# Optimization experiments

Measured on AMD Instinct MI355X. Metric: run time of the kernel, lower is better.

## Reference

```python
import jax, jax.numpy as jnp
import numpy as np

EPS = 1e-09  # present in module but unused in forward math

def setup_inputs() -> dict:
    key = jax.random.key(0)
    k1, k2 = jax.random.split(key)
    n, d = 4096, 512
    outputs = jax.random.normal(k1, (n, d), dtype=jnp.float32)
    labels = jax.random.randint(k2, (n,), 0, 100, dtype=jnp.int64)
    return {"outputs": outputs, "labels": labels, "margin": 1.0}

def reference(outputs, labels, margin):
    # Pairwise squared L2 distances D[i,j] = ||x_i - x_j||^2 via expansion.
    sq = jnp.sum(outputs * outputs, axis=-1)                     # [n]
    D = sq[:, None] + sq[None, :] - 2.0 * (outputs @ outputs.T)  # [n, n]
    D = jnp.maximum(D, 0.0)
    same = (labels[:, None] == labels[None, :])                  # [n, n] bool; includes diagonal
    zn1 = jnp.sum(same)
    zn2 = same.size - zn1
    sum1 = jnp.sum(jnp.where(same, D, 0.0))
    sum2 = jnp.sum(jnp.where(same, 0.0, jnp.maximum(0.0, margin - D)))
    return 0.5 * (sum1 / zn1 + sum2 / zn2)
```

## Files before the change

kernel.cpp:

```cpp
#include <hip/hip_runtime.h>
#include <stdint.h>

#define NROWS 4096
#define DIM   512
#define BK    32
#define TILE  128
#define NBLK  32
#define NPAIR 528

typedef float f32x4 __attribute__((ext_vector_type(4)));
typedef short s16x8 __attribute__((ext_vector_type(8)));

#define OFF_XB   0u
#define OFF_SQ   (NROWS * DIM * 2u)
#define OFF_LAB  (OFF_SQ + NROWS * 4u)
#define OFF_ACC  (OFF_LAB + NROWS * 4u)

__device__ __forceinline__ unsigned short f2bf(float f) {
  unsigned u = __float_as_uint(f);
  return (unsigned short)((u + 0x7FFFu + ((u >> 16) & 1u)) >> 16);
}

typedef __attribute__((address_space(1))) unsigned int glb_uint;
typedef __attribute__((address_space(3))) unsigned int lds_uint;

__device__ __forceinline__ void gl2lds16(const void* g, void* l) {
  __builtin_amdgcn_global_load_lds(
      (glb_uint*)(uintptr_t)g,
      (lds_uint*)(unsigned int)(uintptr_t)l,
      16, 0, 0);
}

__global__ __launch_bounds__(256) void prep_kernel(
    const float* __restrict__ X, const long long* __restrict__ lab,
    unsigned short* __restrict__ Xb, float* __restrict__ sq,
    int* __restrict__ labi, float* __restrict__ accum)
{
  int t = threadIdx.x;
  int gid = blockIdx.x * 256 + t;
  if (gid < 4) accum[gid] = 0.0f;
  if (gid < NROWS) labi[gid] = (int)lab[gid];

  int wave = t >> 6, lane = t & 63;
  int row = blockIdx.x * 4 + wave;
  const float4* Xr = (const float4*)(X + (size_t)row * DIM);
  float4 a = Xr[lane * 2];
  float4 b = Xr[lane * 2 + 1];

  uint4 pk;
  pk.x = (unsigned)f2bf(a.x) | ((unsigned)f2bf(a.y) << 16);
  pk.y = (unsigned)f2bf(a.z) | ((unsigned)f2bf(a.w) << 16);
  pk.z = (unsigned)f2bf(b.x) | ((unsigned)f2bf(b.y) << 16);
  pk.w = (unsigned)f2bf(b.z) | ((unsigned)f2bf(b.w) << 16);
  *(uint4*)(Xb + (size_t)row * DIM + lane * 8) = pk;

  float s = a.x*a.x + a.y*a.y + a.z*a.z + a.w*a.w
          + b.x*b.x + b.y*b.y + b.z*b.z + b.w*b.w;
  #pragma unroll
  for (int off = 32; off; off >>= 1) s += __shfl_down(s, off, 64);
  if (lane == 0) sq[row] = s;
}

__global__ __launch_bounds__(256) void pair_kernel(
    const unsigned short* __restrict__ Xb, const float* __restrict__ sq,
    const int* __restrict__ labi, const float* __restrict__ marginp,
    float* __restrict__ accum)
{
  __shared__ unsigned short As[TILE * BK];
  __shared__ unsigned short Bs[TILE * BK];
  __shared__ float sRow[TILE], sCol[TILE];
  __shared__ int   lRow[TILE], lCol[TILE];
  __shared__ float rs1[4], rs2[4];
  __shared__ int   rc[4];

  int t = threadIdx.x;

  int rem = blockIdx.x, bi = 0;
  while (rem >= (NBLK - bi)) { rem -= (NBLK - bi); bi++; }
  int bj = bi + rem;

  int wave = t >> 6, lane = t & 63;
  int quad = lane >> 4, ml = lane & 15;
  int waveRow = (wave >> 1) * 64, waveCol = (wave & 1) * 64;

  f32x4 acc[4][4] = {};

  const int r0 = t >> 2;
  const int c0 = (t & 3) * 8;
  const size_t gA0 = (size_t)(bi * TILE +       r0) * DIM + c0;
  const size_t gA1 = (size_t)(bi * TILE + 64 +  r0) * DIM + c0;
  const size_t gB0 = (size_t)(bj * TILE +       r0) * DIM + c0;
  const size_t gB1 = (size_t)(bj * TILE + 64 +  r0) * DIM + c0;

  const s16x8* Ap = (const s16x8*)As;
  const s16x8* Bp = (const s16x8*)Bs;

  for (int kt = 0; kt < DIM / BK; ++kt) {
    __syncthreads();
    size_t ko = (size_t)kt * BK;
    gl2lds16(Xb + gA0 + ko, (void*)(As + t * 8));
    gl2lds16(Xb + gA1 + ko, (void*)(As + 2048 + t * 8));
    gl2lds16(Xb + gB0 + ko, (void*)(Bs + t * 8));
    gl2lds16(Xb + gB1 + ko, (void*)(Bs + 2048 + t * 8));
    __syncthreads();

    s16x8 af[4], bfr[4];
    #pragma unroll
    for (int r = 0; r < 4; ++r)
      af[r] = Ap[(waveRow + r * 16 + ml) * 4 + quad];
    #pragma unroll
    for (int c = 0; c < 4; ++c)
      bfr[c] = Bp[(waveCol + c * 16 + ml) * 4 + quad];

    #pragma unroll
    for (int r = 0; r < 4; ++r)
      #pragma unroll
      for (int c = 0; c < 4; ++c)
        acc[r][c] = __builtin_amdgcn_mfma_f32_16x16x32_bf16(af[r], bfr[c], acc[r][c], 0, 0, 0);
  }

  if (t < TILE) {
    sRow[t] = sq[bi * TILE + t];
    lRow[t] = labi[bi * TILE + t];
  } else {
    int u = t - TILE;
    sCol[u] = sq[bj * TILE + u];
    lCol[u] = labi[bj * TILE + u];
  }
  __syncthreads();

  float margin = *marginp;
  float s1 = 0.f, s2 = 0.f;
  int cnt = 0;
  #pragma unroll
  for (int c = 0; c < 4; ++c) {
    int col = waveCol + c * 16 + ml;
    float sqc = sCol[col];
    int lc = lCol[col];
    #pragma unroll
    for (int r = 0; r < 4; ++r) {
      int rbase = waveRow + r * 16 + quad * 4;
      #pragma unroll
      for (int i = 0; i < 4; ++i) {
        int row = rbase + i;
        float d = sRow[row] + sqc - 2.0f * acc[r][c][i];
        d = fmaxf(d, 0.0f);
        if (lRow[row] == lc) { s1 += d; cnt++; }
        else                 { s2 += fmaxf(margin - d, 0.0f); }
      }
    }
  }

  #pragma unroll
  for (int off = 32; off; off >>= 1) {
    s1  += __shfl_down(s1, off, 64);
    s2  += __shfl_down(s2, off, 64);
    cnt += __shfl_down(cnt, off, 64);
  }
  if (lane == 0) { rs1[wave] = s1; rs2[wave] = s2; rc[wave] = cnt; }
  __syncthreads();
  if (t == 0) {
    float f = (bi == bj) ? 1.f : 2.f;
    float S1 = 0.f, S2 = 0.f;
    int C = 0;
    for (int w = 0; w < 4; ++w) { S1 += rs1[w]; S2 += rs2[w]; C += rc[w]; }
    atomicAdd(&accum[0], S1 * f);
    atomicAdd(&accum[1], S2 * f);
    atomicAdd((unsigned*)accum + 2, (unsigned)C * (unsigned)((bi == bj) ? 1 : 2));
  }
}

__global__ void final_kernel(const float* __restrict__ accum, float* __restrict__ out) {
  unsigned c1 = ((const unsigned*)accum)[2];
  double zn1 = (double)c1;
  double zn2 = (double)NROWS * (double)NROWS - zn1;
  double res = 0.5 * ((double)accum[0] / zn1 + (double)accum[1] / zn2);
  out[0] = (float)res;
}

extern "C" void kernel_launch(void* const* d_in, const int* in_sizes, int n_in,
                              void* d_out, int out_size, void* d_ws, size_t ws_size,
                              hipStream_t stream) {
  const float*     X      = (const float*)d_in[0];
  const long long* lab    = (const long long*)d_in[1];
  const float*     margin = (const float*)d_in[2];
  float*           out    = (float*)d_out;

  char* ws = (char*)d_ws;
  unsigned short* Xb   = (unsigned short*)(ws + OFF_XB);
  float*          sq   = (float*)(ws + OFF_SQ);
  int*            labi = (int*)(ws + OFF_LAB);
  float*          accum= (float*)(ws + OFF_ACC);

  prep_kernel<<<NROWS / 4, 256, 0, stream>>>(X, lab, Xb, sq, labi, accum);
  pair_kernel<<<NPAIR, 256, 0, stream>>>(Xb, sq, labi, margin, accum);
  final_kernel<<<1, 1, 0, stream>>>(accum, out);
}
```

Measured before the change: 98.58 us.

## Double-buffer LDS tiles, swizzle LDS layout, fold final reduction into pair kernel

The pair kernel now double-buffers the A and B LDS tiles, so the global-to-LDS copy for the next K step is issued before the MFMAs on the current step. This drops one barrier per iteration and overlaps load latency with compute. An XOR swizzle on the 16-byte chunk index cuts LDS bank conflicts on fragment reads. The separate final kernel is removed: the last block to finish, detected with an atomic ticket counter, computes the output, which saves one launch at the cost of a threadfence and an extra atomic per block.

```diff
diff --git a/kernel.cpp b/kernel.cpp
--- a/kernel.cpp
+++ b/kernel.cpp
@@ -7,6 +7,7 @@
 #define TILE  128
 #define NBLK  32
 #define NPAIR 528
+#define KT    (DIM / BK)
 
 typedef float f32x4 __attribute__((ext_vector_type(4)));
 typedef short s16x8 __attribute__((ext_vector_type(8)));
@@ -64,10 +65,10 @@
 __global__ __launch_bounds__(256) void pair_kernel(
     const unsigned short* __restrict__ Xb, const float* __restrict__ sq,
     const int* __restrict__ labi, const float* __restrict__ marginp,
-    float* __restrict__ accum)
+    float* __restrict__ accum, float* __restrict__ out)
 {
-  __shared__ unsigned short As[TILE * BK];
-  __shared__ unsigned short Bs[TILE * BK];
+  __shared__ unsigned short As[2][TILE * BK];
+  __shared__ unsigned short Bs[2][TILE * BK];
   __shared__ float sRow[TILE], sCol[TILE];
   __shared__ int   lRow[TILE], lCol[TILE];
   __shared__ float rs1[4], rs2[4];
@@ -78,46 +79,6 @@
   int rem = blockIdx.x, bi = 0;
   while (rem >= (NBLK - bi)) { rem -= (NBLK - bi); bi++; }
   int bj = bi + rem;
-
-  int wave = t >> 6, lane = t & 63;
-  int quad = lane >> 4, ml = lane & 15;
-  int waveRow = (wave >> 1) * 64, waveCol = (wave & 1) * 64;
-
-  f32x4 acc[4][4] = {};
-
-  const int r0 = t >> 2;
-  const int c0 = (t & 3) * 8;
-  const size_t gA0 = (size_t)(bi * TILE +       r0) * DIM + c0;
-  const size_t gA1 = (size_t)(bi * TILE + 64 +  r0) * DIM + c0;
-  const size_t gB0 = (size_t)(bj * TILE +       r0) * DIM + c0;
-  const size_t gB1 = (size_t)(bj * TILE + 64 +  r0) * DIM + c0;
-
-  const s16x8* Ap = (const s16x8*)As;
-  const s16x8* Bp = (const s16x8*)Bs;
-
-  for (int kt = 0; kt < DIM / BK; ++kt) {
-    __syncthreads();
-    size_t ko = (size_t)kt * BK;
-    gl2lds16(Xb + gA0 + ko, (void*)(As + t * 8));
-    gl2lds16(Xb + gA1 + ko, (void*)(As + 2048 + t * 8));
-    gl2lds16(Xb + gB0 + ko, (void*)(Bs + t * 8));
-    gl2lds16(Xb + gB1 + ko, (void*)(Bs + 2048 + t * 8));
-    __syncthreads();
-
-    s16x8 af[4], bfr[4];
-    #pragma unroll
-    for (int r = 0; r < 4; ++r)
-      af[r] = Ap[(waveRow + r * 16 + ml) * 4 + quad];
-    #pragma unroll
-    for (int c = 0; c < 4; ++c)
-      bfr[c] = Bp[(waveCol + c * 16 + ml) * 4 + quad];
-
-    #pragma unroll
-    for (int r = 0; r < 4; ++r)
-      #pragma unroll
-      for (int c = 0; c < 4; ++c)
-        acc[r][c] = __builtin_amdgcn_mfma_f32_16x16x32_bf16(af[r], bfr[c], acc[r][c], 0, 0, 0);
-  }
 
   if (t < TILE) {
     sRow[t] = sq[bi * TILE + t];
@@ -127,7 +88,60 @@
     sCol[u] = sq[bj * TILE + u];
     lCol[u] = labi[bj * TILE + u];
   }
-  __syncthreads();
+
+  int wave = t >> 6, lane = t & 63;
+  int quad = lane >> 4, ml = lane & 15;
+  int waveRow = (wave >> 1) * 64, waveCol = (wave & 1) * 64;
+
+  f32x4 acc[4][4] = {};
+
+  const int r0 = t >> 2;
+  const int g  = (t & 3) ^ ((t >> 3) & 3);
+  const size_t gA0 = (size_t)(bi * TILE +      r0) * DIM + g * 8;
+  const size_t gA1 = (size_t)(bi * TILE + 64 + r0) * DIM + g * 8;
+  const size_t gB0 = (size_t)(bj * TILE +      r0) * DIM + g * 8;
+  const size_t gB1 = (size_t)(bj * TILE + 64 + r0) * DIM + g * 8;
+  const int ldst = t * 8;
+
+  const int slot = quad ^ ((ml >> 1) & 3);
+
+  gl2lds16(Xb + gA0, (void*)(As[0] + ldst));
+  gl2lds16(Xb + gA1, (void*)(As[0] + 2048 + ldst));
+  gl2lds16(Xb + gB0, (void*)(Bs[0] + ldst));
+  gl2lds16(Xb + gB1, (void*)(Bs[0] + 2048 + ldst));
+
+  for (int kt = 0; kt < KT; ++kt) {
+    int cur = kt & 1;
+    __syncthreads();
+
+    if (kt + 1 < KT) {
+      size_t ko = (size_t)(kt + 1) * BK;
+      gl2lds16(Xb + gA0 + ko, (void*)(As[cur ^ 1] + ldst));
+      gl2lds16(Xb + gA1 + ko, (void*)(As[cur ^ 1] + 2048 + ldst));
+      gl2lds16(Xb + gB0 + ko, (void*)(Bs[cur ^ 1] + ldst));
+      gl2lds16(Xb + gB1 + ko, (void*)(Bs[cur ^ 1] + 2048 + ldst));
+    }
+
+    const s16x8* Ap = (const s16x8*)As[cur];
+    const s16x8* Bp = (const s16x8*)Bs[cur];
+    s16x8 af[4], bfr[4];
+    #pragma unroll
+    for (int r = 0; r < 4; ++r) {
+      int row = waveRow + r * 16 + ml;
+      af[r] = Ap[row * 4 + slot];
+    }
+    #pragma unroll
+    for (int c = 0; c < 4; ++c) {
+      int col = waveCol + c * 16 + ml;
+      bfr[c] = Bp[col * 4 + slot];
+    }
+
+    #pragma unroll
+    for (int r = 0; r < 4; ++r)
+      #pragma unroll
+      for (int c = 0; c < 4; ++c)
+        acc[r][c] = __builtin_amdgcn_mfma_f32_16x16x32_bf16(af[r], bfr[c], acc[r][c], 0, 0, 0);
+  }
 
   float margin = *marginp;
   float s1 = 0.f, s2 = 0.f;
@@ -167,15 +181,17 @@
     atomicAdd(&accum[0], S1 * f);
     atomicAdd(&accum[1], S2 * f);
     atomicAdd((unsigned*)accum + 2, (unsigned)C * (unsigned)((bi == bj) ? 1 : 2));
-  }
-}
-
-__global__ void final_kernel(const float* __restrict__ accum, float* __restrict__ out) {
-  unsigned c1 = ((const unsigned*)accum)[2];
-  double zn1 = (double)c1;
-  double zn2 = (double)NROWS * (double)NROWS - zn1;
-  double res = 0.5 * ((double)accum[0] / zn1 + (double)accum[1] / zn2);
-  out[0] = (float)res;
+    __threadfence();
+    unsigned prev = atomicAdd((unsigned*)accum + 3, 1u);
+    if (prev == NPAIR - 1) {
+      float s1v = atomicAdd(&accum[0], 0.0f);
+      float s2v = atomicAdd(&accum[1], 0.0f);
+      unsigned c1 = atomicAdd((unsigned*)accum + 2, 0u);
+      double zn1 = (double)c1;
+      double zn2 = (double)NROWS * (double)NROWS - zn1;
+      out[0] = (float)(0.5 * ((double)s1v / zn1 + (double)s2v / zn2));
+    }
+  }
 }
 
 extern "C" void kernel_launch(void* const* d_in, const int* in_sizes, int n_in,
@@ -193,6 +209,5 @@
   float*          accum= (float*)(ws + OFF_ACC);
 
   prep_kernel<<<NROWS / 4, 256, 0, stream>>>(X, lab, Xb, sq, labi, accum);
-  pair_kernel<<<NPAIR, 256, 0, stream>>>(Xb, sq, labi, margin, accum);
-  final_kernel<<<1, 1, 0, stream>>>(accum, out);
-}
+  pair_kernel<<<NPAIR, 256, 0, stream>>>(Xb, sq, labi, margin, accum, out);
+}
```

Result: slower. 102.8 us (+4.3%).
